# Kernel tuning notes

Hardware: AMD Instinct MI355X
Metric: run time of the kernel (lower is better)

The kernel has to match this reference:

```python
import jax, jax.numpy as jnp
import numpy as np

HIDDEN = 2048
N_HEADS = 8
N_KV_HEADS = 1
HEAD_DIM = 256
ROPE_THETA = 10000.0
B, S = 2, 2048


def setup_inputs() -> dict:
    key = jax.random.key(0)
    ks = jax.random.split(key, 6)
    sc = 0.02
    hidden_states = jax.random.normal(ks[0], (B, S, HIDDEN), dtype=jnp.float32)
    position_ids = jnp.broadcast_to(jnp.arange(S, dtype=jnp.int64 if jax.config.jax_enable_x64 else jnp.int32), (B, S))
    # additive causal mask: 0 on/below diagonal, large negative above
    causal = jnp.tril(jnp.ones((S, S), dtype=bool))
    attention_mask = jnp.where(causal, 0.0, -1e9).astype(jnp.float32)[None, None, :, :]
    attention_mask = jnp.broadcast_to(attention_mask, (B, 1, S, S))
    Wq = jax.random.normal(ks[1], (HIDDEN, N_HEADS * HEAD_DIM), dtype=jnp.float32) * sc
    Wk = jax.random.normal(ks[2], (HIDDEN, N_KV_HEADS * HEAD_DIM), dtype=jnp.float32) * sc
    Wv = jax.random.normal(ks[3], (HIDDEN, N_KV_HEADS * HEAD_DIM), dtype=jnp.float32) * sc
    Wo = jax.random.normal(ks[4], (N_HEADS * HEAD_DIM, HIDDEN), dtype=jnp.float32) * sc
    return {"hidden_states": hidden_states, "position_ids": position_ids,
            "attention_mask": attention_mask, "Wq": Wq, "Wk": Wk, "Wv": Wv, "Wo": Wo}


def _rotate_half(x):
    x1, x2 = jnp.split(x, 2, axis=-1)
    return jnp.concatenate([-x2, x1], axis=-1)


def _rope_cos_sin(position_ids, dtype):
    # inv_freq: [head_dim/2]
    inv_freq = 1.0 / (ROPE_THETA ** (jnp.arange(0, HEAD_DIM, 2, dtype=jnp.float32) / HEAD_DIM))
    # freqs: [B, S, head_dim/2]
    freqs = position_ids.astype(jnp.float32)[:, :, None] * inv_freq[None, None, :]
    emb = jnp.concatenate([freqs, freqs], axis=-1)  # [B, S, head_dim]
    return jnp.cos(emb).astype(dtype), jnp.sin(emb).astype(dtype)


def reference(hidden_states, position_ids, attention_mask, Wq, Wk, Wv, Wo):
    b, s, _ = hidden_states.shape
    # projections (bias=False)
    q = (hidden_states @ Wq).reshape(b, s, N_HEADS, HEAD_DIM).transpose(0, 2, 1, 3)      # [B,H,S,D]
    k = (hidden_states @ Wk).reshape(b, s, N_KV_HEADS, HEAD_DIM).transpose(0, 2, 1, 3)   # [B,Hk,S,D]
    v = (hidden_states @ Wv).reshape(b, s, N_KV_HEADS, HEAD_DIM).transpose(0, 2, 1, 3)
    cos, sin = _rope_cos_sin(position_ids, hidden_states.dtype)  # [B,S,D]
    cos, sin = cos[:, None], sin[:, None]  # [B,1,S,D]
    q = q * cos + _rotate_half(q) * sin
    k = k * cos + _rotate_half(k) * sin
    # repeat_kv for GQA
    n_rep = N_HEADS // N_KV_HEADS
    k = jnp.repeat(k, n_rep, axis=1)  # [B,H,S,D]
    v = jnp.repeat(v, n_rep, axis=1)
    scale = HEAD_DIM ** -0.5
    scores = jnp.einsum('bhqd,bhkd->bhqk', q, k) * scale + attention_mask
    attn_weights = jax.nn.softmax(scores.astype(jnp.float32), axis=-1).astype(q.dtype)
    attn_out = jnp.einsum('bhqk,bhkd->bhqd', attn_weights, v)
    attn_out = attn_out.transpose(0, 2, 1, 3).reshape(b, s, N_HEADS * HEAD_DIM)
    out = attn_out @ Wo
    return out, attn_weights
```

## Files before the change

kernel.cpp:

```cpp
#include <hip/hip_runtime.h>
#include <hip/hip_bf16.h>
#include <math.h>

typedef __attribute__((ext_vector_type(4))) float f32x4;
typedef __attribute__((ext_vector_type(8))) __bf16 bf16x8;
typedef __attribute__((ext_vector_type(8))) unsigned short u16x8;
typedef __attribute__((ext_vector_type(4))) unsigned short u16x4;

#define HID    2048
#define NHEADS 8
#define HDIM   256
#define SEQ    2048
#define BATCH  2
#define ROWS   (BATCH*SEQ)
#define QKVN   (NHEADS*HDIM + 2*HDIM)
#define NBH    (BATCH*NHEADS)

typedef __attribute__((address_space(1))) const void gvoid_t;
typedef __attribute__((address_space(3))) void lvoid_t;

__device__ __forceinline__ void gload16(const void* g, void* l){
  __builtin_amdgcn_global_load_lds((gvoid_t*)g, (lvoid_t*)l, 16, 0, 0);
}

__device__ __forceinline__ float bf2f(unsigned short u){
  union { unsigned int i; float f; } x; x.i = ((unsigned int)u) << 16; return x.f;
}
__device__ __forceinline__ unsigned short f2bf(float f){
  union { float f; unsigned int i; } x; x.f = f;
  unsigned int u = x.i;
  return (unsigned short)((u + 0x7FFFu + ((u >> 16) & 1u)) >> 16);
}

__global__ __launch_bounds__(256)
void k_f32_to_bf16(const float* __restrict__ src, unsigned short* __restrict__ dst){
  long i = ((long)blockIdx.x * 256 + threadIdx.x) * 16;
  f32x4 x0 = *(const f32x4*)(src + i);
  f32x4 x1 = *(const f32x4*)(src + i + 4);
  f32x4 x2 = *(const f32x4*)(src + i + 8);
  f32x4 x3 = *(const f32x4*)(src + i + 12);
  u16x8 w0, w1;
  #pragma unroll
  for (int j = 0; j < 4; ++j){
    w0[j]   = f2bf(x0[j]);
    w0[4+j] = f2bf(x1[j]);
    w1[j]   = f2bf(x2[j]);
    w1[4+j] = f2bf(x3[j]);
  }
  *(u16x8*)(dst + i)     = w0;
  *(u16x8*)(dst + i + 8) = w1;
}

__global__ __launch_bounds__(256)
void k_transpose(const float* __restrict__ src, unsigned short* __restrict__ dst,
                 int srcCols, int dstLd){
  __shared__ float t[32][33];
  int bx = blockIdx.x * 32;
  int by = blockIdx.y * 32;
  int tx = threadIdx.x & 31, ty = threadIdx.x >> 5;
  #pragma unroll
  for (int i = 0; i < 4; ++i){
    int rr = ty + i*8;
    t[rr][tx] = src[(long)(by + rr)*srcCols + bx + tx];
  }
  __syncthreads();
  #pragma unroll
  for (int i = 0; i < 4; ++i){
    int rr = ty + i*8;
    dst[(long)(bx + rr)*dstLd + by + tx] = f2bf(t[tx][rr]);
  }
}

__global__ __launch_bounds__(256)
void k_rope(const unsigned short* __restrict__ qkv, const int* __restrict__ pos_ids,
            unsigned short* __restrict__ Qb, unsigned short* __restrict__ Kb){
  int row = blockIdx.x;
  float pos = (float)pos_ids[row];
  int tid = threadIdx.x;
  const unsigned short* r = qkv + (long)row * QKVN;

  #pragma unroll
  for (int it = 0; it < 4; ++it){
    int p = it*256 + tid;
    int d = p & 127, h = p >> 7;
    int col = h*HDIM + d;
    float inv = exp2f((float)d * -0.10381025296523132f);
    float ang = pos * inv;
    float sn, cs; sincosf(ang, &sn, &cs);
    float x0 = bf2f(r[col]), x1 = bf2f(r[col + 128]);
    Qb[(long)row*HID + col]       = f2bf(x0*cs - x1*sn);
    Qb[(long)row*HID + col + 128] = f2bf(x1*cs + x0*sn);
  }
  if (tid < 128){
    int d = tid;
    float inv = exp2f((float)d * -0.10381025296523132f);
    float ang = pos * inv;
    float sn, cs; sincosf(ang, &sn, &cs);
    float x0 = bf2f(r[HID + d]), x1 = bf2f(r[HID + d + 128]);
    Kb[(long)row*HDIM + d]       = f2bf(x0*cs - x1*sn);
    Kb[(long)row*HDIM + d + 128] = f2bf(x1*cs + x0*sn);
  }
}

__global__ __launch_bounds__(256)
void k_vt(const unsigned short* __restrict__ qkvb, unsigned short* __restrict__ VT){
  __shared__ unsigned short t[32][34];
  int d0 = blockIdx.x * 32, s0 = blockIdx.y * 32, b = blockIdx.z;
  int tx = threadIdx.x & 31, ty = threadIdx.x >> 5;
  #pragma unroll
  for (int i = 0; i < 4; ++i){
    int rr = ty + i*8;
    t[rr][tx] = qkvb[(long)(b*SEQ + s0 + rr)*QKVN + HID + HDIM + d0 + tx];
  }
  __syncthreads();
  #pragma unroll
  for (int i = 0; i < 4; ++i){
    int dd = ty + i*8;
    VT[((long)b*HDIM + d0 + dd)*SEQ + s0 + tx] = t[tx][dd];
  }
}

__global__ __launch_bounds__(512, 4)
void k_fused(const unsigned short* __restrict__ Qb, const unsigned short* __restrict__ Kb,
             const unsigned short* __restrict__ VT, float* __restrict__ S,
             unsigned short* __restrict__ AOb){
  int bh = blockIdx.x, b = bh >> 3, h = bh & 7;
  int ss = 31 - (int)blockIdx.y;
  int qbase = ss * 64;
  int T = 2 * (ss + 1);

  float* Sh = S + (long)bh * SEQ * SEQ;
  const unsigned short* Qh = Qb + (long)b*SEQ*HID + (long)h*HDIM;
  const unsigned short* Kh = Kb + (long)b*SEQ*HDIM;
  const unsigned short* Vh = VT + (long)b*HDIM*SEQ;

  __shared__ unsigned short lK[2][32*256];
  __shared__ unsigned short lA[2][64*40];
  __shared__ float lWl[8][64];
  __shared__ float mli[64];

  int tid = threadIdx.x, lane = tid & 63, w = tid >> 6;
  int wr = w >> 1, wc = w & 1;

#define STAGE_K(kt_, buf_)                                                      \
  { _Pragma("unroll")                                                           \
    for (int t = 0; t < 2; ++t){                                                \
      int seg = w*2 + t;                                                        \
      int row = seg*2 + (lane >> 5);                                            \
      int cb  = ((lane & 31)*16) ^ ((row & 7) << 4);                            \
      gload16(Kh + (long)((kt_)*32 + row)*HDIM + (cb >> 1),                     \
              (char*)lK[buf_] + seg*1024);                                      \
    } }

#define QKT(buf_)                                                               \
  { _Pragma("unroll")                                                           \
    for (int kk = 0; kk < 8; ++kk){                                             \
      int rk = wc*16 + (lane & 15);                                             \
      bf16x8 bk = *(const bf16x8*)((const char*)lK[buf_] + rk*512 +             \
                   ((kk*64 + (lane >> 4)*16) ^ ((rk & 7) << 4)));               \
      accs = __builtin_amdgcn_mfma_f32_16x16x32_bf16(aq[kk], bk, accs, 0, 0, 0);\
    } }

  bf16x8 aq[8];
  {
    const unsigned short* qrow = Qh + (long)(qbase + wr*16 + (lane & 15))*HID + (lane >> 4)*8;
    #pragma unroll
    for (int kk = 0; kk < 8; ++kk)
      aq[kk] = *(const bf16x8*)(qrow + kk*32);
  }

  f32x4 accs;
  f32x4 acc_o[4][2];
  float oL[4];
  #pragma unroll
  for (int q = 0; q < 4; ++q){ accs[q] = 0.f; oL[q] = 0.f; }
  #pragma unroll
  for (int m = 0; m < 4; ++m)
    #pragma unroll
    for (int n = 0; n < 2; ++n)
      #pragma unroll
      for (int q = 0; q < 4; ++q) acc_o[m][n][q] = 0.f;

  STAGE_K(0, 0)
  STAGE_K(1, 1)
  asm volatile("s_waitcnt vmcnt(2)" ::: "memory");
  __builtin_amdgcn_s_barrier();
  for (int kt = 0; kt < T; ++kt){
    __builtin_amdgcn_s_setprio(1);
    QKT(kt & 1)
    __builtin_amdgcn_s_setprio(0);
    #pragma unroll
    for (int ri = 0; ri < 4; ++ri){
      int rowl = wr*16 + (lane >> 4)*4 + ri;
      int coll = wc*16 + (lane & 15);
      float e = (kt*32 + coll <= qbase + rowl) ? __expf(accs[ri]*0.0625f - 8.0f) : 0.f;
      oL[ri] += e;
      lA[kt & 1][rowl*40 + coll] = f2bf(e);
      accs[ri] = 0.f;
    }
    bf16x8 vf0 = *(const bf16x8*)(Vh + (long)(w*32 +      (lane & 15))*SEQ + kt*32 + (lane >> 4)*8);
    bf16x8 vf1 = *(const bf16x8*)(Vh + (long)(w*32 + 16 + (lane & 15))*SEQ + kt*32 + (lane >> 4)*8);
    asm volatile("s_waitcnt lgkmcnt(0)" ::: "memory");
    asm volatile("s_waitcnt vmcnt(2)" ::: "memory");
    __builtin_amdgcn_s_barrier();
    if (kt + 2 < T) STAGE_K(kt + 2, kt & 1)
    __builtin_amdgcn_s_setprio(1);
    #pragma unroll
    for (int m2 = 0; m2 < 4; ++m2){
      int rq = m2*16 + (lane & 15);
      bf16x8 ap = *(const bf16x8*)&lA[kt & 1][rq*40 + (lane >> 4)*8];
      acc_o[m2][0] = __builtin_amdgcn_mfma_f32_16x16x32_bf16(ap, vf0, acc_o[m2][0], 0, 0, 0);
      acc_o[m2][1] = __builtin_amdgcn_mfma_f32_16x16x32_bf16(ap, vf1, acc_o[m2][1], 0, 0, 0);
    }
    __builtin_amdgcn_s_setprio(0);
  }

  #pragma unroll
  for (int ri = 0; ri < 4; ++ri){
    float v = oL[ri];
    #pragma unroll
    for (int off = 1; off < 16; off <<= 1) v += __shfl_xor(v, off);
    if ((lane & 15) == 0)
      lWl[w][wr*16 + (lane >> 4)*4 + ri] = v;
  }
  __syncthreads();
  if (tid < 64){
    int g = (tid >> 4) * 2;
    mli[tid] = 1.0f / (lWl[g][tid] + lWl[g+1][tid]);
  }
  __syncthreads();

  float ils[4];
  #pragma unroll
  for (int ri = 0; ri < 4; ++ri)
    ils[ri] = mli[wr*16 + (lane >> 4)*4 + ri];

  #pragma unroll
  for (int m2 = 0; m2 < 4; ++m2){
    #pragma unroll
    for (int ri = 0; ri < 4; ++ri){
      int row = m2*16 + (lane >> 4)*4 + ri;
      float il = mli[row];
      long gr = (long)b*SEQ + qbase + row;
      #pragma unroll
      for (int n = 0; n < 2; ++n){
        int col = w*32 + n*16 + (lane & 15);
        AOb[gr*HID + h*HDIM + col] = f2bf(acc_o[m2][n][ri] * il);
      }
    }
  }

  STAGE_K(0, 0)
  STAGE_K(1, 1)
  asm volatile("s_waitcnt vmcnt(2)" ::: "memory");
  __builtin_amdgcn_s_barrier();
  for (int kt = 0; kt < T; ++kt){
    __builtin_amdgcn_s_setprio(1);
    QKT(kt & 1)
    __builtin_amdgcn_s_setprio(0);
    #pragma unroll
    for (int ri = 0; ri < 4; ++ri){
      int rowl = wr*16 + (lane >> 4)*4 + ri;
      int coll = wc*16 + (lane & 15);
      float p = (kt*32 + coll <= qbase + rowl)
                ? __expf(accs[ri]*0.0625f - 8.0f) * ils[ri] : 0.f;
      Sh[(long)(qbase + rowl)*SEQ + kt*32 + coll] = p;
      accs[ri] = 0.f;
    }
    asm volatile("s_waitcnt vmcnt(4)" ::: "memory");
    __builtin_amdgcn_s_barrier();
    if (kt + 2 < T) STAGE_K(kt + 2, kt & 1)
  }

  {
    f32x4 z4; z4[0]=0.f; z4[1]=0.f; z4[2]=0.f; z4[3]=0.f;
    int row = qbase + (tid >> 3);
    for (int c = T*32 + (tid & 7)*4; c < SEQ; c += 32)
      *(f32x4*)&Sh[(long)row*SEQ + c] = z4;
  }
#undef STAGE_K
#undef QKT
}

template<int OUTF32>
__global__ __launch_bounds__(512, 1)
void gemm256(const unsigned short* __restrict__ A16, const unsigned short* __restrict__ BT,
             void* __restrict__ Cv, int lda, int ldb, int ldc, int K){
  constexpr int BM = 256, BN = 128, BK = 64;
  int m0 = blockIdx.x * BM, n0 = blockIdx.y * BN;

  __shared__ unsigned short lA[2][BM*BK];
  __shared__ unsigned short lB[2][BN*BK];

  int tid = threadIdx.x, lane = tid & 63, w = tid >> 6;
  int wr = w >> 1, wc = w & 1;
  int srow = lane >> 3;
  int vswz = ((lane & 7) ^ ((lane >> 3) & 7)) * 8;

  f32x4 acc[4][4];
  #pragma unroll
  for (int m = 0; m < 4; ++m)
    #pragma unroll
    for (int n = 0; n < 4; ++n)
      #pragma unroll
      for (int q = 0; q < 4; ++q) acc[m][n][q] = 0.f;

  int NT = K / BK;

#define STAGE256(kt_, buf_)                                                    \
  { int k0_ = (kt_) * BK;                                                      \
    _Pragma("unroll")                                                          \
    for (int t = 0; t < 4; ++t){                                               \
      int seg = w*4 + t;                                                       \
      const unsigned short* src = A16 + (long)(m0 + seg*8 + srow)*lda + k0_ + vswz; \
      gload16(src, (char*)lA[buf_] + seg*1024);                                \
    }                                                                          \
    _Pragma("unroll")                                                          \
    for (int t = 0; t < 2; ++t){                                               \
      int seg = w*2 + t;                                                       \
      const unsigned short* src = BT + (long)(n0 + seg*8 + srow)*ldb + k0_ + vswz; \
      gload16(src, (char*)lB[buf_] + seg*1024);                                \
    } }

  STAGE256(0, 0)
  STAGE256(1, 1)
  int cur = 0;

  for (int kt = 0; kt < NT; ++kt){
    if (kt < NT - 1) asm volatile("s_waitcnt vmcnt(6)" ::: "memory");
    else             asm volatile("s_waitcnt vmcnt(0)" ::: "memory");
    __builtin_amdgcn_s_barrier();

    const char* La = (const char*)lA[cur];
    const char* Lb = (const char*)lB[cur];
    __builtin_amdgcn_s_setprio(1);
    #pragma unroll
    for (int kk = 0; kk < 2; ++kk){
      bf16x8 af[4], bfr[4];
      #pragma unroll
      for (int m = 0; m < 4; ++m){
        int row = wr*64 + m*16 + (lane & 15);
        int kb = (kk*64 + (lane >> 4)*16) ^ ((row & 7) << 4);
        af[m] = *(const bf16x8*)(La + row*128 + kb);
      }
      #pragma unroll
      for (int n = 0; n < 4; ++n){
        int row = wc*64 + n*16 + (lane & 15);
        int kb = (kk*64 + (lane >> 4)*16) ^ ((row & 7) << 4);
        bfr[n] = *(const bf16x8*)(Lb + row*128 + kb);
      }
      #pragma unroll
      for (int m = 0; m < 4; ++m)
        #pragma unroll
        for (int n = 0; n < 4; ++n)
          acc[m][n] = __builtin_amdgcn_mfma_f32_16x16x32_bf16(af[m], bfr[n], acc[m][n], 0, 0, 0);
    }
    __builtin_amdgcn_s_setprio(0);
    __builtin_amdgcn_s_barrier();
    if (kt + 2 < NT) STAGE256(kt + 2, cur)
    cur ^= 1;
  }
#undef STAGE256

  #pragma unroll
  for (int m = 0; m < 4; ++m){
    #pragma unroll
    for (int ri = 0; ri < 4; ++ri){
      int orow = m0 + wr*64 + m*16 + (lane >> 4)*4 + ri;
      #pragma unroll
      for (int n = 0; n < 4; ++n){
        int ocol = n0 + wc*64 + n*16 + (lane & 15);
        float vv = acc[m][n][ri];
        if (OUTF32) ((float*)Cv)[(long)orow*ldc + ocol] = vv;
        else        ((unsigned short*)Cv)[(long)orow*ldc + ocol] = f2bf(vv);
      }
    }
  }
}

extern "C" void kernel_launch(void* const* d_in, const int* in_sizes, int n_in,
                              void* d_out, int out_size, void* d_ws, size_t ws_size,
                              hipStream_t stream){
  const float* hs  = (const float*)d_in[0];
  const int*   pos = (const int*)  d_in[1];
  const float* Wq  = (const float*)d_in[3];
  const float* Wk  = (const float*)d_in[4];
  const float* Wv  = (const float*)d_in[5];
  const float* Wo  = (const float*)d_in[6];

  float* out  = (float*)d_out;
  float* Sbuf = out + (long)ROWS * HID;

  unsigned short* wsp   = (unsigned short*)d_ws;
  unsigned short* hsb   = wsp;
  unsigned short* wqkvT = hsb   + (long)ROWS*HID;
  unsigned short* woT   = wqkvT + (long)QKVN*HID;
  unsigned short* qkvb  = woT   + (long)HID*HID;
  unsigned short* Qb    = qkvb  + (long)ROWS*QKVN;
  unsigned short* Kb    = Qb    + (long)ROWS*HID;
  unsigned short* VT    = Kb    + (long)ROWS*HDIM;
  unsigned short* AOb   = VT    + (long)BATCH*HDIM*SEQ;

  k_f32_to_bf16<<<(ROWS*HID)/(256*16), 256, 0, stream>>>(hs, hsb);
  k_transpose<<<dim3(HID/32,  HID/32), 256, 0, stream>>>(Wq, wqkvT, HID, HID);
  k_transpose<<<dim3(HDIM/32, HID/32), 256, 0, stream>>>(Wk, wqkvT + (long)HID*HID, HDIM, HID);
  k_transpose<<<dim3(HDIM/32, HID/32), 256, 0, stream>>>(Wv, wqkvT + (long)(HID+HDIM)*HID, HDIM, HID);
  k_transpose<<<dim3(HID/32,  HID/32), 256, 0, stream>>>(Wo, woT, HID, HID);

  gemm256<0><<<dim3(ROWS/256, QKVN/128), 512, 0, stream>>>(
      hsb, wqkvT, qkvb, HID, HID, QKVN, HID);

  k_rope<<<ROWS, 256, 0, stream>>>(qkvb, pos, Qb, Kb);
  k_vt<<<dim3(HDIM/32, SEQ/32, BATCH), 256, 0, stream>>>(qkvb, VT);

  k_fused<<<dim3(NBH, 32), 512, 0, stream>>>(Qb, Kb, VT, Sbuf, AOb);

  gemm256<1><<<dim3(ROWS/256, HID/128), 512, 0, stream>>>(
      AOb, woT, out, HID, HID, HID, HID);
}
```

Before: 318.3 us.

## Triple-buffer GEMM LDS and interleave prefetch with MFMA phases

Moves the 256x128 GEMM from double to triple LDS buffering. Each k-tile is split into four phases, and each phase interleaves LDS fragment reads, a slice of the global-to-LDS prefetch for tile j+2, and 8 MFMAs. This removes the trailing barrier-then-stage bubble and spreads memory issue across compute. It adds more barriers per tile and raises LDS use to 144KB, which is safe only because launch bounds already force one block per CU.

```diff
diff --git a/kernel.cpp b/kernel.cpp
--- a/kernel.cpp
+++ b/kernel.cpp
@@ -289,8 +289,8 @@
   constexpr int BM = 256, BN = 128, BK = 64;
   int m0 = blockIdx.x * BM, n0 = blockIdx.y * BN;
 
-  __shared__ unsigned short lA[2][BM*BK];
-  __shared__ unsigned short lB[2][BN*BK];
+  __shared__ unsigned short lA[3][BM*BK];
+  __shared__ unsigned short lB[3][BN*BK];
 
   int tid = threadIdx.x, lane = tid & 63, w = tid >> 6;
   int wr = w >> 1, wc = w & 1;
@@ -307,60 +307,81 @@
 
   int NT = K / BK;
 
-#define STAGE256(kt_, buf_)                                                    \
-  { int k0_ = (kt_) * BK;                                                      \
-    _Pragma("unroll")                                                          \
-    for (int t = 0; t < 4; ++t){                                               \
-      int seg = w*4 + t;                                                       \
-      const unsigned short* src = A16 + (long)(m0 + seg*8 + srow)*lda + k0_ + vswz; \
-      gload16(src, (char*)lA[buf_] + seg*1024);                                \
-    }                                                                          \
-    _Pragma("unroll")                                                          \
-    for (int t = 0; t < 2; ++t){                                               \
-      int seg = w*2 + t;                                                       \
-      const unsigned short* src = BT + (long)(n0 + seg*8 + srow)*ldb + k0_ + vswz; \
-      gload16(src, (char*)lB[buf_] + seg*1024);                                \
+#define STG_A(kt_, buf_, t_)                                                   \
+  { int seg = w*4 + (t_);                                                      \
+    gload16(A16 + (long)(m0 + seg*8 + srow)*lda + (kt_)*BK + vswz,             \
+            (char*)lA[buf_] + seg*1024); }
+#define STG_B(kt_, buf_, t_)                                                   \
+  { int seg = w*2 + (t_);                                                      \
+    gload16(BT + (long)(n0 + seg*8 + srow)*ldb + (kt_)*BK + vswz,              \
+            (char*)lB[buf_] + seg*1024); }
+#define RD_A(mh_, kk_, buf_)                                                   \
+  { _Pragma("unroll")                                                          \
+    for (int mi = 0; mi < 2; ++mi){                                            \
+      int row = wr*64 + ((mh_)*2 + mi)*16 + (lane & 15);                       \
+      af[mi] = *(const bf16x8*)((const char*)lA[buf_] + row*128 +              \
+                 (((kk_)*64 + (lane >> 4)*16) ^ ((row & 7) << 4)));            \
     } }
-
-  STAGE256(0, 0)
-  STAGE256(1, 1)
+#define RD_B(kk_, buf_)                                                        \
+  { _Pragma("unroll")                                                          \
+    for (int n = 0; n < 4; ++n){                                               \
+      int row = wc*64 + n*16 + (lane & 15);                                    \
+      bfr[n] = *(const bf16x8*)((const char*)lB[buf_] + row*128 +              \
+                 (((kk_)*64 + (lane >> 4)*16) ^ ((row & 7) << 4)));            \
+    } }
+#define MFMA8(mh_)                                                             \
+  { _Pragma("unroll")                                                          \
+    for (int mi = 0; mi < 2; ++mi)                                             \
+      _Pragma("unroll")                                                        \
+      for (int n = 0; n < 4; ++n)                                              \
+        acc[(mh_)*2 + mi][n] = __builtin_amdgcn_mfma_f32_16x16x32_bf16(        \
+            af[mi], bfr[n], acc[(mh_)*2 + mi][n], 0, 0, 0); }
+#define PH_SYNC                                                                \
+  __builtin_amdgcn_s_barrier();                                                \
+  asm volatile("s_waitcnt lgkmcnt(0)" ::: "memory");
+
+  STG_A(0,0,0) STG_A(0,0,1) STG_A(0,0,2) STG_A(0,0,3) STG_B(0,0,0) STG_B(0,0,1)
+  STG_A(1,1,0) STG_A(1,1,1) STG_A(1,1,2) STG_A(1,1,3) STG_B(1,1,0) STG_B(1,1,1)
+  asm volatile("s_waitcnt vmcnt(6)" ::: "memory");
+  __builtin_amdgcn_s_barrier();
+
   int cur = 0;
-
-  for (int kt = 0; kt < NT; ++kt){
-    if (kt < NT - 1) asm volatile("s_waitcnt vmcnt(6)" ::: "memory");
-    else             asm volatile("s_waitcnt vmcnt(0)" ::: "memory");
-    __builtin_amdgcn_s_barrier();
-
-    const char* La = (const char*)lA[cur];
-    const char* Lb = (const char*)lB[cur];
-    __builtin_amdgcn_s_setprio(1);
-    #pragma unroll
-    for (int kk = 0; kk < 2; ++kk){
-      bf16x8 af[4], bfr[4];
-      #pragma unroll
-      for (int m = 0; m < 4; ++m){
-        int row = wr*64 + m*16 + (lane & 15);
-        int kb = (kk*64 + (lane >> 4)*16) ^ ((row & 7) << 4);
-        af[m] = *(const bf16x8*)(La + row*128 + kb);
-      }
-      #pragma unroll
-      for (int n = 0; n < 4; ++n){
-        int row = wc*64 + n*16 + (lane & 15);
-        int kb = (kk*64 + (lane >> 4)*16) ^ ((row & 7) << 4);
-        bfr[n] = *(const bf16x8*)(Lb + row*128 + kb);
-      }
-      #pragma unroll
-      for (int m = 0; m < 4; ++m)
-        #pragma unroll
-        for (int n = 0; n < 4; ++n)
-          acc[m][n] = __builtin_amdgcn_mfma_f32_16x16x32_bf16(af[m], bfr[n], acc[m][n], 0, 0, 0);
-    }
-    __builtin_amdgcn_s_setprio(0);
-    __builtin_amdgcn_s_barrier();
-    if (kt + 2 < NT) STAGE256(kt + 2, cur)
-    cur ^= 1;
-  }
-#undef STAGE256
+  for (int j = 0; j < NT; ++j){
+    int fut = cur + 2; if (fut >= 3) fut -= 3;
+    bool pf = (j + 2 < NT);
+    bf16x8 af[2], bfr[4];
+
+    RD_A(0, 0, cur) RD_B(0, cur)
+    if (pf){ STG_A(j+2, fut, 0) STG_A(j+2, fut, 1) }
+    PH_SYNC
+    __builtin_amdgcn_s_setprio(1); MFMA8(0) __builtin_amdgcn_s_setprio(0);
+    __builtin_amdgcn_s_barrier();
+    RD_A(1, 0, cur)
+    if (pf){ STG_A(j+2, fut, 2) STG_A(j+2, fut, 3) }
+    PH_SYNC
+    __builtin_amdgcn_s_setprio(1); MFMA8(1) __builtin_amdgcn_s_setprio(0);
+    __builtin_amdgcn_s_barrier();
+    RD_A(0, 1, cur) RD_B(1, cur)
+    if (pf){ STG_B(j+2, fut, 0) }
+    PH_SYNC
+    __builtin_amdgcn_s_setprio(1); MFMA8(0) __builtin_amdgcn_s_setprio(0);
+    __builtin_amdgcn_s_barrier();
+    RD_A(1, 1, cur)
+    if (pf){ STG_B(j+2, fut, 1) }
+    if (pf) asm volatile("s_waitcnt vmcnt(6)" ::: "memory");
+    else    asm volatile("s_waitcnt vmcnt(0)" ::: "memory");
+    PH_SYNC
+    __builtin_amdgcn_s_setprio(1); MFMA8(1) __builtin_amdgcn_s_setprio(0);
+    __builtin_amdgcn_s_barrier();
+
+    cur += 1; if (cur >= 3) cur -= 3;
+  }
+#undef STG_A
+#undef STG_B
+#undef RD_A
+#undef RD_B
+#undef MFMA8
+#undef PH_SYNC
 
   #pragma unroll
   for (int m = 0; m < 4; ++m){
```

New measurement: 335.6 us. 1.05x slower.
